# Performance work log

Hardware: AMD Instinct MI355X
Metric: run time of the kernel (lower is better)

Reference implementation:

```python
import jax, jax.numpy as jnp
import numpy as np

K = 16  # top-k neighbors
P = 2.0  # norm order (Euclidean)


def setup_inputs() -> dict:
    key = jax.random.key(0)
    k1, k2 = jax.random.split(key)
    keys = jax.random.normal(k1, (8192, 64), dtype=jnp.float32)
    queries = jax.random.normal(k2, (32768, 64), dtype=jnp.float32)
    return {"keys": keys, "queries": queries}


def _pairwise_sq_dists(a, b):
    # ||a-b||^2 = ||a||^2 + ||b||^2 - 2 a.b ; [Na, Nb]
    a2 = jnp.sum(a * a, axis=1)[:, None]
    b2 = jnp.sum(b * b, axis=1)[None, :]
    return a2 + b2 - 2.0 * (a @ b.T)


def reference(keys, queries):
    # Exact kNN: index is built over `queries`, searched with `keys`
    # (mirrors index.add(queries); index.search(keys, k)).
    d2 = _pairwise_sq_dists(keys, queries)          # [Nk, Nq]
    neg_top, indices = jax.lax.top_k(-d2, K)        # smallest distances
    # Differentiable-path distance recomputation (pnorm, p=2, root=False):
    gathered = queries[indices]                     # [Nk, K, d]
    diffs = jnp.abs(keys[:, None, :] - gathered)
    distances = jnp.sum(diffs ** P, axis=-1)        # squared L2 (root=False)
    return indices, distances
```

## Files before the change

kernel.cpp:

```cpp
#include <hip/hip_runtime.h>
#include <hip/hip_bf16.h>
#include <cfloat>
#include <climits>

#define DDIM 64
#define KSEL 16
#define WINDOW 4096
#define NCHUNK 64
#define C1 0.017f
#define C2 0.05f
#define RFAST 1024
#define RBUF 1040
#define LSLOT 32

typedef __attribute__((ext_vector_type(8))) short short8;
typedef __attribute__((ext_vector_type(4))) float f32x4;

__device__ __forceinline__ float np_sum64(const float* p) {
  float lane[16];
#pragma unroll
  for (int j = 0; j < 16; ++j)
    lane[j] = __fadd_rn(__fadd_rn(p[j], p[16 + j]),
                        __fadd_rn(p[32 + j], p[48 + j]));
  float u[8];
#pragma unroll
  for (int j = 0; j < 8; ++j) u[j] = __fadd_rn(lane[j], lane[j + 8]);
  float w[4];
#pragma unroll
  for (int j = 0; j < 4; ++j) w[j] = __fadd_rn(u[j], u[j + 4]);
  return __fadd_rn(__fadd_rn(w[0], w[2]), __fadd_rn(w[1], w[3]));
}

__device__ __forceinline__ void insert16(float* bd, int* bi, float cd, int ci) {
#pragma unroll
  for (int p = 0; p < KSEL; ++p) {
    bool sm = (cd < bd[p]) || (cd == bd[p] && ci < bi[p]);
    float td = bd[p]; int ti = bi[p];
    bd[p] = sm ? cd : td; bi[p] = sm ? ci : ti;
    cd = sm ? td : cd;   ci = sm ? ti : ci;
  }
}

__device__ __forceinline__ unsigned long long packdj(float d, int j) {
  unsigned db = __float_as_uint(d);
  db = (db & 0x80000000u) ? ~db : (db | 0x80000000u);
  return ((unsigned long long)db << 32) | (unsigned)j;
}

__device__ __forceinline__ unsigned mapmono(float d) {
  unsigned db = __float_as_uint(d);
  return (db & 0x80000000u) ? ~db : (db | 0x80000000u);
}

__device__ __forceinline__ float unmapmono(unsigned m) {
  return (m & 0x80000000u) ? __uint_as_float(m & 0x7fffffffu)
                           : __uint_as_float(~m);
}

__device__ __forceinline__ float exact_d2(const float* __restrict__ k,
                                          const float* __restrict__ q,
                                          float k2, float q2) {
  float c = 0.f;
#pragma unroll
  for (int t = 0; t < DDIM; ++t) c = fmaf(k[t], q[t], c);
  return __fsub_rn(__fadd_rn(k2, q2), __fmul_rn(2.0f, c));
}

__device__ __forceinline__ unsigned bf2pack(float a, float b) {
  __hip_bfloat16 ha = __float2bfloat16(a), hb = __float2bfloat16(b);
  unsigned short ua = *reinterpret_cast<unsigned short*>(&ha);
  unsigned short ub = *reinterpret_cast<unsigned short*>(&hb);
  return (unsigned)ua | ((unsigned)ub << 16);
}

__device__ __forceinline__ unsigned short bf_down(float x) {
  unsigned u = __float_as_uint(x);
  unsigned short hs = (unsigned short)(u >> 16);
  if ((u & 0xFFFFu) && x < 0.0f) hs += 1;
  return hs;
}
__device__ __forceinline__ unsigned short bf_up(float x) {
  unsigned u = __float_as_uint(x);
  unsigned short hs = (unsigned short)(u >> 16);
  if ((u & 0xFFFFu) && x > 0.0f) hs += 1;
  return hs;
}
__device__ __forceinline__ float bf_val(unsigned short h) {
  return __uint_as_float(((unsigned)h) << 16);
}

__global__ __launch_bounds__(256) void knn_norms_np(
    const float* __restrict__ keys, const float* __restrict__ queries,
    int Nk, int Nq, float* __restrict__ k2, float* __restrict__ q2,
    float* __restrict__ sk, float* __restrict__ sq,
    unsigned short* __restrict__ kbf, unsigned short* __restrict__ qbf,
    unsigned short* __restrict__ QE8) {
  int i = blockIdx.x * 256 + threadIdx.x;
  if (i >= Nk + Nq) return;
  bool isK = i < Nk;
  int r = isK ? i : i - Nk;
  const float4* row4 = reinterpret_cast<const float4*>(
      (isK ? keys : queries) + (size_t)r * DDIM);
  float p[DDIM]; unsigned hw[DDIM / 2];
#pragma unroll
  for (int t = 0; t < 16; ++t) {
    float4 v = row4[t];
    p[4 * t + 0] = __fmul_rn(v.x, v.x);
    p[4 * t + 1] = __fmul_rn(v.y, v.y);
    p[4 * t + 2] = __fmul_rn(v.z, v.z);
    p[4 * t + 3] = __fmul_rn(v.w, v.w);
    hw[2 * t + 0] = bf2pack(v.x, v.y);
    hw[2 * t + 1] = bf2pack(v.z, v.w);
  }
  float s = np_sum64(p);
  uint4* dst = reinterpret_cast<uint4*>((isK ? kbf : qbf) + (size_t)r * DDIM);
#pragma unroll
  for (int t = 0; t < 8; ++t)
    dst[t] = make_uint4(hw[4 * t], hw[4 * t + 1], hw[4 * t + 2], hw[4 * t + 3]);
  if (isK) { k2[r] = s; sk[r] = sqrtf(s); }
  else {
    q2[r] = s;
    float sv = sqrtf(s);
    sq[r] = sv;
    float h = 0.5f * s;
    unsigned short hhi = bf_down(h);
    float rem = h - bf_val(hhi);
    unsigned short hlo = (rem > 0.f) ? bf_down(rem) : (unsigned short)0;
    unsigned short e[8] = {0x3F80, bf_up(sv), hhi, hlo, 0, 0, 0, 0};
    uint4* qe = reinterpret_cast<uint4*>(QE8 + (size_t)r * 8);
    *qe = make_uint4((unsigned)e[0] | ((unsigned)e[1] << 16),
                     (unsigned)e[2] | ((unsigned)e[3] << 16), 0u, 0u);
  }
}

__global__ __launch_bounds__(256) void knn_init(
    unsigned* __restrict__ cmin, int nmin,
    unsigned* __restrict__ cnt, int ncnt) {
  int i = blockIdx.x * 256 + threadIdx.x;
  if (i < nmin) cmin[i] = 0xFFFFFFFFu;
  if (i < ncnt) cnt[i] = 0u;
}

__global__ __launch_bounds__(256) void knn_chunkmin(
    const unsigned short* __restrict__ kbf, const unsigned short* __restrict__ qbf,
    const float* __restrict__ k2a, const float* __restrict__ ska,
    const float* __restrict__ q2a, const float* __restrict__ sqa,
    unsigned* __restrict__ cmin) {
  int tid = threadIdx.x, lane = tid & 63, w = tid >> 6;
  int kb = blockIdx.x & 127;
  int qt = blockIdx.x >> 7;
  int kbase = kb * 64;
  int qbase = qt * 256 + w * 64;
  int chunk = qbase >> 6;
  int l16 = lane & 15, lg = lane >> 4;

  short8 a0[4], a1[4];
#pragma unroll
  for (int s = 0; s < 4; ++s) {
    const short8* krow = reinterpret_cast<const short8*>(
        kbf + (size_t)(kbase + s * 16 + l16) * DDIM);
    a0[s] = krow[lg]; a1[s] = krow[lg + 4];
  }
  float KA[16], KB[16];
#pragma unroll
  for (int s = 0; s < 4; ++s)
#pragma unroll
    for (int r = 0; r < 4; ++r) {
      int kk = kbase + s * 16 + lg * 4 + r;
      KA[s * 4 + r] = k2a[kk] + C2;
      KB[s * 4 + r] = C1 * ska[kk];
    }
  float mreg[16];
#pragma unroll
  for (int i = 0; i < 16; ++i) mreg[i] = FLT_MAX;

#pragma unroll
  for (int qs = 0; qs < 4; ++qs) {
    int q = qbase + qs * 16 + l16;
    const short8* qrow = reinterpret_cast<const short8*>(qbf + (size_t)q * DDIM);
    short8 b0 = qrow[lg], b1 = qrow[lg + 4];
    float q2l = q2a[q], sql = sqa[q];
    f32x4 acc[4];
#pragma unroll
    for (int s = 0; s < 4; ++s) {
      f32x4 z = {0.f, 0.f, 0.f, 0.f};
      z = __builtin_amdgcn_mfma_f32_16x16x32_bf16(a0[s], b0, z, 0, 0, 0);
      z = __builtin_amdgcn_mfma_f32_16x16x32_bf16(a1[s], b1, z, 0, 0, 0);
      acc[s] = z;
    }
#pragma unroll
    for (int s = 0; s < 4; ++s)
#pragma unroll
      for (int r = 0; r < 4; ++r) {
        int i = s * 4 + r;
        float u = fmaf(KB[i], sql, KA[i] + q2l) - 2.0f * acc[s][r];
        mreg[i] = fminf(mreg[i], u);
      }
  }
#pragma unroll
  for (int m = 1; m < 16; m <<= 1)
#pragma unroll
    for (int i = 0; i < 16; ++i)
      mreg[i] = fminf(mreg[i], __shfl_xor(mreg[i], m));
  if (l16 == 0) {
#pragma unroll
    for (int i = 0; i < 16; ++i) {
      int kk = kbase + (i >> 2) * 16 + lg * 4 + (i & 3);
      atomicMin(&cmin[(size_t)kk * NCHUNK + chunk], mapmono(mreg[i]));
    }
  }
}

__global__ __launch_bounds__(256) void knn_thresh3(
    const unsigned* __restrict__ cmin,
    const float* __restrict__ k2a, const float* __restrict__ ska,
    int Nk, unsigned short* __restrict__ KE8) {
  int key = blockIdx.x * 256 + threadIdx.x;
  if (key >= Nk) return;
  unsigned b[KSEL];
#pragma unroll
  for (int p = 0; p < KSEL; ++p) b[p] = 0xFFFFFFFFu;
  const unsigned* row = cmin + (size_t)key * NCHUNK;
  for (int c = 0; c < NCHUNK; ++c) {
    unsigned v = row[c];
    if (v < b[KSEL - 1]) {
      unsigned cv = v;
#pragma unroll
      for (int p = 0; p < KSEL; ++p) {
        bool sm = cv < b[p];
        unsigned t = b[p];
        b[p] = sm ? cv : t;
        cv = sm ? t : cv;
      }
    }
  }
  float T = unmapmono(b[KSEL - 1]);
  float psA = 0.5f * (k2a[key] - T - C2);
  float psB = -0.5f * C1 * ska[key];
  unsigned short e0 = (unsigned short)(bf_down(psA) ^ 0x8000);
  unsigned short e1 = (unsigned short)(bf_down(psB) ^ 0x8000);
  uint4* ke = reinterpret_cast<uint4*>(KE8 + (size_t)key * 8);
  *ke = make_uint4((unsigned)e0 | ((unsigned)e1 << 16),
                   0xBF80u | (0xBF80u << 16), 0u, 0u);
}

__global__ __launch_bounds__(256) void knn_filter(
    const unsigned short* __restrict__ kbf, const unsigned short* __restrict__ qbf,
    const unsigned short* __restrict__ KE8, const unsigned short* __restrict__ QE8,
    unsigned* __restrict__ cnt, unsigned short* __restrict__ cbuf, int CAP) {
  __shared__ int lcnt[64];
  __shared__ int lbase[64];
  __shared__ unsigned short lhit[64 * LSLOT];
  int tid = threadIdx.x;
  int lane = tid & 63, w = tid >> 6;
  int kb = blockIdx.x & 127;
  int qt = blockIdx.x >> 7;
  int kbase = kb * 64;
  int qwave = qt * 1024 + w * 256;
  int l16 = lane & 15, lg = lane >> 4;
  const short8 z8 = {0, 0, 0, 0, 0, 0, 0, 0};

  if (tid < 64) lcnt[tid] = 0;
  __syncthreads();

  short8 a0[4], a1[4], a2[4];
#pragma unroll
  for (int s = 0; s < 4; ++s) {
    const short8* krow = reinterpret_cast<const short8*>(
        kbf + (size_t)(kbase + s * 16 + l16) * DDIM);
    a0[s] = krow[lg]; a1[s] = krow[lg + 4];
    a2[s] = (lg == 0)
        ? *reinterpret_cast<const short8*>(KE8 + (size_t)(kbase + s * 16 + l16) * 8)
        : z8;
  }

  for (int qo = 0; qo < 4; ++qo) {
    int qbase = qwave + qo * 64;
#pragma unroll
    for (int qs = 0; qs < 4; ++qs) {
      int q = qbase + qs * 16 + l16;
      const short8* qrow = reinterpret_cast<const short8*>(qbf + (size_t)q * DDIM);
      short8 b0 = qrow[lg], b1 = qrow[lg + 4];
      short8 b2 = (lg == 0)
          ? *reinterpret_cast<const short8*>(QE8 + (size_t)q * 8)
          : z8;

      f32x4 acc[4];
#pragma unroll
      for (int s = 0; s < 4; ++s) {
        f32x4 z = {0.f, 0.f, 0.f, 0.f};
        z = __builtin_amdgcn_mfma_f32_16x16x32_bf16(a0[s], b0, z, 0, 0, 0);
        z = __builtin_amdgcn_mfma_f32_16x16x32_bf16(a1[s], b1, z, 0, 0, 0);
        z = __builtin_amdgcn_mfma_f32_16x16x32_bf16(a2[s], b2, z, 0, 0, 0);
        acc[s] = z;
      }
      unsigned m = 0;
#pragma unroll
      for (int s = 0; s < 4; ++s)
#pragma unroll
        for (int r = 0; r < 4; ++r)
          m |= (acc[s][r] > 0.0f) ? (1u << (s * 4 + r)) : 0u;
      while (m) {
        int b = __ffs(m) - 1; m &= m - 1;
        int kl = (b >> 2) * 16 + lg * 4 + (b & 3);
        int slot = atomicAdd(&lcnt[kl], 1);
        if (slot < LSLOT) lhit[kl * LSLOT + slot] = (unsigned short)q;
      }
    }
  }
  __syncthreads();
  if (tid < 64) {
    int lc = lcnt[tid];
    int key = kbase + tid;
    unsigned add = (lc > LSLOT) ? (unsigned)(CAP + 1000) : (unsigned)lc;
    lbase[tid] = (lc > 0) ? (int)atomicAdd(&cnt[key], add) : 0;
    lcnt[tid] = lc < LSLOT ? lc : LSLOT;
  }
  __syncthreads();
  for (int idx = tid; idx < 64 * LSLOT; idx += 256) {
    int kl = idx >> 5, sl = idx & (LSLOT - 1);
    if (sl < lcnt[kl]) {
      int pos = lbase[kl] + sl;
      if (pos < CAP)
        cbuf[(size_t)(kbase + kl) * CAP + pos] = lhit[kl * LSLOT + sl];
    }
  }
}

__global__ __launch_bounds__(256) void knn_recheck(
    const float* __restrict__ keys, const float* __restrict__ queries,
    const float* __restrict__ k2a, const float* __restrict__ q2a,
    const unsigned* __restrict__ cnt, const unsigned short* __restrict__ cbuf,
    int CAP, int Nq, float* __restrict__ outIdx) {
  __shared__ unsigned long long packs[RBUF];
  __shared__ unsigned long long cur16[KSEL];
  __shared__ float4 klds[16];
  int tid = threadIdx.x;
  int key = blockIdx.x;
  float myk2 = k2a[key];

  if (tid < 16)
    klds[tid] = reinterpret_cast<const float4*>(keys + (size_t)key * DDIM)[tid];
  __syncthreads();

  unsigned n = cnt[key];
  unsigned lim = (unsigned)((CAP < RFAST) ? CAP : RFAST);
  if (n <= lim) {
    const unsigned short* mc = cbuf + (size_t)key * CAP;
    int sub = tid & 3;
    int lanebase = (tid & 63) & ~3;
    for (unsigned base = 0; base < n; base += 64) {
      unsigned e = base + (unsigned)(tid >> 2);
      unsigned ec = (e < n) ? e : (n - 1);
      int j = mc[ec];
      const float4* Q = reinterpret_cast<const float4*>(queries + (size_t)j * DDIM);
      float4 rr[4];
      rr[0] = Q[sub];
      rr[1] = Q[sub + 4];
      rr[2] = Q[sub + 8];
      rr[3] = Q[sub + 12];
      float q2j = q2a[j];
      float c = 0.f;
#pragma unroll
      for (int seg = 0; seg < 16; ++seg) {
        float4 kk = klds[seg];
        float4 qq = rr[seg >> 2];
        float t = c;
        t = fmaf(kk.x, qq.x, t);
        t = fmaf(kk.y, qq.y, t);
        t = fmaf(kk.z, qq.z, t);
        t = fmaf(kk.w, qq.w, t);
        c = __shfl(t, lanebase + (seg & 3), 64);
      }
      if (e < n && sub == 0) {
        float d2 = __fsub_rn(__fadd_rn(myk2, q2j), __fmul_rn(2.0f, c));
        packs[e] = packdj(d2, j);
      }
    }
    __syncthreads();
    int N = (int)n;
    for (int i = tid; i < N; i += 256) {
      unsigned long long mp = packs[i];
      int c = 0;
      for (int m = 0; m < N; ++m) c += packs[m] < mp;
      if (c < KSEL)
        outIdx[(size_t)key * KSEL + c] = (float)(int)(mp & 0xFFFFFFFFull);
    }
    return;
  }

  float bd[KSEL]; int bi[KSEL];
#pragma unroll
  for (int p = 0; p < KSEL; ++p) { bd[p] = FLT_MAX; bi[p] = INT_MAX; }
  const float* krow = keys + (size_t)key * DDIM;
  for (int j = tid; j < Nq; j += 256) {
    float d2 = exact_d2(krow, queries + (size_t)j * DDIM, myk2, q2a[j]);
    if (d2 < bd[KSEL - 1] || (d2 == bd[KSEL - 1] && j < bi[KSEL - 1]))
      insert16(bd, bi, d2, j);
  }
  if (tid < KSEL) cur16[tid] = ~0ull;
  __syncthreads();
  for (int r = 0; r < 4; ++r) {
    if ((tid >> 6) == r) {
#pragma unroll
      for (int p = 0; p < KSEL; ++p)
        packs[KSEL + (tid & 63) * KSEL + p] = packdj(bd[p], bi[p]);
    }
    if (tid < KSEL) packs[tid] = cur16[tid];
    __syncthreads();
    const int N = KSEL + 64 * KSEL;
    for (int i = tid; i < N; i += 256) {
      unsigned long long mp = packs[i];
      int c = 0;
      for (int m = 0; m < N; ++m) c += packs[m] < mp;
      if (c < KSEL) cur16[c] = mp;
    }
    __syncthreads();
  }
  if (tid < KSEL)
    outIdx[(size_t)key * KSEL + tid] =
        (float)(int)(cur16[tid] & 0xFFFFFFFFull);
}

__global__ __launch_bounds__(256) void knn_dist_d(
    const float* __restrict__ keys, const float* __restrict__ queries,
    const float* __restrict__ outIdx, int Nk, float* __restrict__ outDist) {
  int e = blockIdx.x * 256 + threadIdx.x;
  if (e >= Nk * KSEL) return;
  int key = e >> 4;
  int id = (int)outIdx[e];
  const float* kp = keys + (size_t)key * DDIM;
  const float* qp = queries + (size_t)id * DDIM;
  double s = 0.0;
#pragma unroll
  for (int t = 0; t < DDIM; ++t) {
    double d = (double)kp[t] - (double)qp[t];
    s = fma(d, d, s);
  }
  outDist[e] = (float)s;
}

extern "C" void kernel_launch(void* const* d_in, const int* in_sizes, int n_in,
                              void* d_out, int out_size, void* d_ws, size_t ws_size,
                              hipStream_t stream) {
  const float* keys    = (const float*)d_in[0];
  const float* queries = (const float*)d_in[1];
  int Nk = in_sizes[0] / DDIM;
  int Nq = in_sizes[1] / DDIM;
  float* out = (float*)d_out;

  char* wp = (char*)d_ws;
  float*    k2  = (float*)wp;  wp += (size_t)Nk * 4;
  float*    q2  = (float*)wp;  wp += (size_t)Nq * 4;
  float*    sk  = (float*)wp;  wp += (size_t)Nk * 4;
  float*    sq  = (float*)wp;  wp += (size_t)Nq * 4;
  unsigned* cnt = (unsigned*)wp; wp += (size_t)Nk * 4;
  unsigned* cmin = (unsigned*)wp; wp += (size_t)Nk * NCHUNK * 4;
  unsigned short* kbf = (unsigned short*)wp; wp += (size_t)Nk * DDIM * 2;
  unsigned short* qbf = (unsigned short*)wp; wp += (size_t)Nq * DDIM * 2;
  unsigned short* KE8 = (unsigned short*)wp; wp += (size_t)Nk * 8 * 2;
  unsigned short* QE8 = (unsigned short*)wp; wp += (size_t)Nq * 8 * 2;
  size_t fixedBytes = (size_t)(wp - (char*)d_ws);
  unsigned short* cbuf = (unsigned short*)wp;
  long long rem = (long long)ws_size - (long long)fixedBytes;
  int CAP = (int)(rem / (2 * (long long)Nk));
  if (CAP > 2048) CAP = 2048;
  if (CAP < 16) CAP = 16;

  int nmin = Nk * NCHUNK;
  knn_init<<<(nmin + 255) / 256, 256, 0, stream>>>(cmin, nmin, cnt, Nk);
  knn_norms_np<<<(Nk + Nq + 255) / 256, 256, 0, stream>>>(
      keys, queries, Nk, Nq, k2, q2, sk, sq, kbf, qbf, QE8);
  knn_chunkmin<<<128 * (WINDOW / 256), 256, 0, stream>>>(
      kbf, qbf, k2, sk, q2, sq, cmin);
  knn_thresh3<<<(Nk + 255) / 256, 256, 0, stream>>>(cmin, k2, sk, Nk, KE8);
  knn_filter<<<128 * (Nq / 1024), 256, 0, stream>>>(
      kbf, qbf, KE8, QE8, cnt, cbuf, CAP);
  knn_recheck<<<Nk, 256, 0, stream>>>(
      keys, queries, k2, q2, cnt, cbuf, CAP, Nq, out);
  knn_dist_d<<<(Nk * KSEL + 255) / 256, 256, 0, stream>>>(
      keys, queries, out, Nk, out + (size_t)Nk * KSEL);
}
```

Measured before the change: 252.3 us.

## Fuse distance recompute into recheck, drop init kernel and chunk-min atomics

Computes the final double-precision distances inside knn_recheck, right after each winning index is chosen, and reuses the key row already staged in shared memory. This removes the separate knn_dist_d launch. The cnt zeroing moves into knn_norms_np, which removes the knn_init launch. The atomicMin on cmin becomes a plain store, which is valid only because each (key, chunk) slot is written by exactly one wave. The aim is fewer launches, no init pass and no atomic traffic, at the cost of extra serial fp64 work inside recheck threads.

```diff
diff --git a/kernel.cpp b/kernel.cpp
--- a/kernel.cpp
+++ b/kernel.cpp
@@ -89,14 +89,30 @@
   return __uint_as_float(((unsigned)h) << 16);
 }
 
+__device__ __forceinline__ float fused_dist(const float4* __restrict__ klds,
+                                            const float* __restrict__ qp) {
+  const float4* q4 = reinterpret_cast<const float4*>(qp);
+  double s = 0.0;
+#pragma unroll
+  for (int t = 0; t < 16; ++t) {
+    float4 kk = klds[t], qv = q4[t];
+    double d0 = (double)kk.x - (double)qv.x; s = fma(d0, d0, s);
+    double d1 = (double)kk.y - (double)qv.y; s = fma(d1, d1, s);
+    double d2 = (double)kk.z - (double)qv.z; s = fma(d2, d2, s);
+    double d3 = (double)kk.w - (double)qv.w; s = fma(d3, d3, s);
+  }
+  return (float)s;
+}
+
 __global__ __launch_bounds__(256) void knn_norms_np(
     const float* __restrict__ keys, const float* __restrict__ queries,
     int Nk, int Nq, float* __restrict__ k2, float* __restrict__ q2,
     float* __restrict__ sk, float* __restrict__ sq,
     unsigned short* __restrict__ kbf, unsigned short* __restrict__ qbf,
-    unsigned short* __restrict__ QE8) {
+    unsigned short* __restrict__ QE8, unsigned* __restrict__ cnt) {
   int i = blockIdx.x * 256 + threadIdx.x;
   if (i >= Nk + Nq) return;
+  if (i < Nk) cnt[i] = 0u;
   bool isK = i < Nk;
   int r = isK ? i : i - Nk;
   const float4* row4 = reinterpret_cast<const float4*>(
@@ -133,14 +149,6 @@
   }
 }
 
-__global__ __launch_bounds__(256) void knn_init(
-    unsigned* __restrict__ cmin, int nmin,
-    unsigned* __restrict__ cnt, int ncnt) {
-  int i = blockIdx.x * 256 + threadIdx.x;
-  if (i < nmin) cmin[i] = 0xFFFFFFFFu;
-  if (i < ncnt) cnt[i] = 0u;
-}
-
 __global__ __launch_bounds__(256) void knn_chunkmin(
     const unsigned short* __restrict__ kbf, const unsigned short* __restrict__ qbf,
     const float* __restrict__ k2a, const float* __restrict__ ska,
@@ -206,7 +214,7 @@
 #pragma unroll
     for (int i = 0; i < 16; ++i) {
       int kk = kbase + (i >> 2) * 16 + lg * 4 + (i & 3);
-      atomicMin(&cmin[(size_t)kk * NCHUNK + chunk], mapmono(mreg[i]));
+      cmin[(size_t)kk * NCHUNK + chunk] = mapmono(mreg[i]);
     }
   }
 }
@@ -331,7 +339,7 @@
     const float* __restrict__ keys, const float* __restrict__ queries,
     const float* __restrict__ k2a, const float* __restrict__ q2a,
     const unsigned* __restrict__ cnt, const unsigned short* __restrict__ cbuf,
-    int CAP, int Nq, float* __restrict__ outIdx) {
+    int CAP, int Nq, float* __restrict__ outIdx, float* __restrict__ outDist) {
   __shared__ unsigned long long packs[RBUF];
   __shared__ unsigned long long cur16[KSEL];
   __shared__ float4 klds[16];
@@ -383,8 +391,12 @@
       unsigned long long mp = packs[i];
       int c = 0;
       for (int m = 0; m < N; ++m) c += packs[m] < mp;
-      if (c < KSEL)
-        outIdx[(size_t)key * KSEL + c] = (float)(int)(mp & 0xFFFFFFFFull);
+      if (c < KSEL) {
+        int j = (int)(mp & 0xFFFFFFFFull);
+        outIdx[(size_t)key * KSEL + c] = (float)j;
+        outDist[(size_t)key * KSEL + c] =
+            fused_dist(klds, queries + (size_t)j * DDIM);
+      }
     }
     return;
   }
@@ -417,27 +429,12 @@
     }
     __syncthreads();
   }
-  if (tid < KSEL)
-    outIdx[(size_t)key * KSEL + tid] =
-        (float)(int)(cur16[tid] & 0xFFFFFFFFull);
-}
-
-__global__ __launch_bounds__(256) void knn_dist_d(
-    const float* __restrict__ keys, const float* __restrict__ queries,
-    const float* __restrict__ outIdx, int Nk, float* __restrict__ outDist) {
-  int e = blockIdx.x * 256 + threadIdx.x;
-  if (e >= Nk * KSEL) return;
-  int key = e >> 4;
-  int id = (int)outIdx[e];
-  const float* kp = keys + (size_t)key * DDIM;
-  const float* qp = queries + (size_t)id * DDIM;
-  double s = 0.0;
-#pragma unroll
-  for (int t = 0; t < DDIM; ++t) {
-    double d = (double)kp[t] - (double)qp[t];
-    s = fma(d, d, s);
-  }
-  outDist[e] = (float)s;
+  if (tid < KSEL) {
+    int j = (int)(cur16[tid] & 0xFFFFFFFFull);
+    outIdx[(size_t)key * KSEL + tid] = (float)j;
+    outDist[(size_t)key * KSEL + tid] =
+        fused_dist(klds, queries + (size_t)j * DDIM);
+  }
 }
 
 extern "C" void kernel_launch(void* const* d_in, const int* in_sizes, int n_in,
@@ -467,17 +464,13 @@
   if (CAP > 2048) CAP = 2048;
   if (CAP < 16) CAP = 16;
 
-  int nmin = Nk * NCHUNK;
-  knn_init<<<(nmin + 255) / 256, 256, 0, stream>>>(cmin, nmin, cnt, Nk);
   knn_norms_np<<<(Nk + Nq + 255) / 256, 256, 0, stream>>>(
-      keys, queries, Nk, Nq, k2, q2, sk, sq, kbf, qbf, QE8);
+      keys, queries, Nk, Nq, k2, q2, sk, sq, kbf, qbf, QE8, cnt);
   knn_chunkmin<<<128 * (WINDOW / 256), 256, 0, stream>>>(
       kbf, qbf, k2, sk, q2, sq, cmin);
   knn_thresh3<<<(Nk + 255) / 256, 256, 0, stream>>>(cmin, k2, sk, Nk, KE8);
   knn_filter<<<128 * (Nq / 1024), 256, 0, stream>>>(
       kbf, qbf, KE8, QE8, cnt, cbuf, CAP);
   knn_recheck<<<Nk, 256, 0, stream>>>(
-      keys, queries, k2, q2, cnt, cbuf, CAP, Nq, out);
-  knn_dist_d<<<(Nk * KSEL + 255) / 256, 256, 0, stream>>>(
-      keys, queries, out, Nk, out + (size_t)Nk * KSEL);
-}
+      keys, queries, k2, q2, cnt, cbuf, CAP, Nq, out, out + (size_t)Nk * KSEL);
+}
```

Measured after the change: 296.5 us. +17.5%, slower.
